# Performance work log

Hardware: AMD Instinct MI355X
Metric: run time of the kernel (lower is better)

## Reference

```python
import jax, jax.numpy as jnp
import numpy as np

EPS = 1e-12  # torch F.normalize eps

N, C, H, W = 64, 512, 40, 40
K = 64  # num_clusters


def setup_inputs() -> dict:
    key = jax.random.key(0)
    k1, k2, k3 = jax.random.split(key, 3)
    x = jax.random.normal(k1, (N, C, H, W), dtype=jnp.float32)
    conv_w = jax.random.normal(k2, (K, C, 1, 1), dtype=jnp.float32) * 0.05
    centroids = jax.random.uniform(k3, (K, C), dtype=jnp.float32)
    return {"x": x, "conv_w": conv_w, "centroids": centroids}


def _l2norm(v, axis):
    return v / jnp.maximum(jnp.sqrt(jnp.sum(v * v, axis=axis, keepdims=True)), EPS)


def reference(x, conv_w, centroids):
    n, c = x.shape[:2]
    k = conv_w.shape[0]
    # descriptor-wise L2 normalization over channels
    xn = _l2norm(x, axis=1)
    xf = xn.reshape(n, c, -1)  # [N, C, P]
    # 1x1 conv (no bias, vladv2=False) == per-pixel matmul with [K, C]
    logits = jnp.einsum('kc,ncp->nkp', conv_w.reshape(k, c), xf)
    a = jax.nn.softmax(logits, axis=1)  # soft assignment over clusters
    # VLAD: sum_p a[n,k,p] * (x[n,:,p] - centroid[k])  (weights are all-ones)
    vlad = jnp.einsum('nkp,ncp->nkc', a, xf) - a.sum(axis=-1)[:, :, None] * centroids[None]
    # intra-normalization over C, flatten, global L2 norm
    vlad = _l2norm(vlad, axis=2).reshape(n, -1)
    vlad = _l2norm(vlad, axis=1)
    return vlad
```

## Files before the change

kernel.cpp:

```cpp
#include <hip/hip_runtime.h>
#include <math.h>

#define EPSF 1e-12f


typedef short bf16x8 __attribute__((ext_vector_type(8)));
typedef float f32x4  __attribute__((ext_vector_type(4)));

__device__ __forceinline__ ushort f2b(float x) {
    unsigned u = __float_as_uint(x);
    return (ushort)((u + 0x7fffu + ((u >> 16) & 1u)) >> 16);
}

__global__ __launch_bounds__(256) void k0_wb(const float* __restrict__ W,
                                             ushort* __restrict__ Wb) {
    int i = blockIdx.x * 256 + threadIdx.x;
    if (i < 64 * 512) Wb[i] = f2b(W[i]);
}

__global__ __launch_bounds__(256) void k1_transpose(const float* __restrict__ x,
                                                    ushort* __restrict__ xbt,
                                                    float* __restrict__ rn) {
    const int n = blockIdx.y, p0 = blockIdx.x * 16;
    const int tid = threadIdx.x;
    __shared__ float tile[512 * 17];
    __shared__ float ssred[16 * 17];
    {
        const int cr = tid >> 2, pc4 = tid & 3;
        const float* src = x + ((size_t)n * 512 + cr) * 1600 + p0 + pc4 * 4;
        #pragma unroll
        for (int it = 0; it < 8; it++) {
            float4 v = *(const float4*)(src + (size_t)it * 64 * 1600);
            float* d = &tile[(cr + it * 64) * 17 + pc4 * 4];
            d[0] = v.x; d[1] = v.y; d[2] = v.z; d[3] = v.w;
        }
    }
    __syncthreads();
    {
        const int pl = tid >> 4, cc = tid & 15;
        float ss = 0.f;
        ushort buf[32] __attribute__((aligned(16)));
        #pragma unroll
        for (int i = 0; i < 32; i++) {
            float v = tile[(cc * 32 + i) * 17 + pl];
            ss = fmaf(v, v, ss);
            buf[i] = f2b(v);
        }
        ushort* dst = xbt + ((size_t)n * 1600 + p0 + pl) * 512 + cc * 32;
        #pragma unroll
        for (int ch = 0; ch < 4; ch++)
            ((uint4*)dst)[ch] = ((const uint4*)buf)[ch];
        ssred[pl * 17 + cc] = ss;
    }
    __syncthreads();
    if (tid < 16) {
        float s = 0.f;
        #pragma unroll
        for (int i = 0; i < 16; i++) s += ssred[tid * 17 + i];
        rn[n * 1600 + p0 + tid] = 1.f / fmaxf(sqrtf(s), EPSF);
    }
}

__global__ __launch_bounds__(256) void k2a_gemm1(const ushort* __restrict__ xbt,
                                                 const ushort* __restrict__ Wb,
                                                 const float* __restrict__ rn,
                                                 ushort* __restrict__ a_t,
                                                 float* __restrict__ asum) {
    const int n = blockIdx.y;
    const int p0 = blockIdx.x * 64;
    const int wv = threadIdx.x >> 6, lane = threadIdx.x & 63;
    const int q = lane >> 4, l15 = lane & 15;
    const int pw = p0 + wv * 16;

    const ushort* arow = xbt + ((size_t)n * 1600 + pw + l15) * 512 + q * 8;
    const ushort* brow = Wb + l15 * 512 + q * 8;

    f32x4 acc[4] = {};
    for (int kc = 0; kc < 512; kc += 32) {
        bf16x8 af = *(const bf16x8*)(arow + kc);
        #pragma unroll
        for (int nt = 0; nt < 4; nt++) {
            bf16x8 bf = *(const bf16x8*)(brow + nt * 16 * 512 + kc);
            acc[nt] = __builtin_amdgcn_mfma_f32_16x16x32_bf16(af, bf, acc[nt], 0, 0, 0);
        }
    }

    float rnv[4];
    #pragma unroll
    for (int r = 0; r < 4; r++) rnv[r] = rn[n * 1600 + pw + q * 4 + r];

    float v[4][4];
    float mx[4] = {-3.4e38f, -3.4e38f, -3.4e38f, -3.4e38f};
    #pragma unroll
    for (int nt = 0; nt < 4; nt++)
        #pragma unroll
        for (int r = 0; r < 4; r++) {
            v[nt][r] = acc[nt][r] * rnv[r];
            mx[r] = fmaxf(mx[r], v[nt][r]);
        }
    #pragma unroll
    for (int s = 1; s <= 8; s <<= 1)
        #pragma unroll
        for (int r = 0; r < 4; r++) mx[r] = fmaxf(mx[r], __shfl_xor(mx[r], s, 64));
    float sm[4] = {0.f, 0.f, 0.f, 0.f};
    #pragma unroll
    for (int nt = 0; nt < 4; nt++)
        #pragma unroll
        for (int r = 0; r < 4; r++) { v[nt][r] = __expf(v[nt][r] - mx[r]); sm[r] += v[nt][r]; }
    #pragma unroll
    for (int s = 1; s <= 8; s <<= 1)
        #pragma unroll
        for (int r = 0; r < 4; r++) sm[r] += __shfl_xor(sm[r], s, 64);
    float inv[4];
    #pragma unroll
    for (int r = 0; r < 4; r++) inv[r] = 1.f / sm[r];
    #pragma unroll
    for (int nt = 0; nt < 4; nt++)
        #pragma unroll
        for (int r = 0; r < 4; r++) v[nt][r] *= inv[r];

    #pragma unroll
    for (int nt = 0; nt < 4; nt++) {
        float t = v[nt][0] + v[nt][1] + v[nt][2] + v[nt][3];
        t += __shfl_xor(t, 16, 64);
        t += __shfl_xor(t, 32, 64);
        if (lane < 16) atomicAdd(&asum[n * 64 + nt * 16 + lane], t);
    }

    __shared__ ushort abuf[4][64 * 24];
    #pragma unroll
    for (int nt = 0; nt < 4; nt++)
        #pragma unroll
        for (int r = 0; r < 4; r++)
            abuf[wv][(nt * 16 + l15) * 24 + q * 4 + r] = f2b(v[nt][r] * rnv[r]);
    __syncthreads();
    ushort* dst = a_t + ((size_t)n * 64 + lane) * 1600 + pw;
    const ushort* srcl = &abuf[wv][lane * 24];
    *(uint4*)(dst)     = *(const uint4*)(srcl);
    *(uint4*)(dst + 8) = *(const uint4*)(srcl + 8);
}

__global__ __launch_bounds__(256) void k3_gemm2(const ushort* __restrict__ a_t,
                                                const float* __restrict__ x,
                                                float* __restrict__ out) {
    const int n = blockIdx.y;
    const int c0 = blockIdx.x * 256;
    const int p0 = blockIdx.z * 320;
    const int wv = threadIdx.x >> 6, lane = threadIdx.x & 63;
    const int q = lane >> 4, l15 = lane & 15;
    const int cw = c0 + wv * 64;

    const ushort* abase = a_t + ((size_t)n * 64 + l15) * 1600 + p0 + q * 8;
    const float*  xbase = x + ((size_t)n * 512 + cw + l15) * 1600 + p0 + q * 8;

    f32x4 acc[4][4] = {};
    for (int pc = 0; pc < 320; pc += 32) {
        bf16x8 af[4];
        #pragma unroll
        for (int mt = 0; mt < 4; mt++)
            af[mt] = *(const bf16x8*)(abase + (size_t)mt * 16 * 1600 + pc);
        bf16x8 bf[4];
        #pragma unroll
        for (int nt = 0; nt < 4; nt++) {
            const float* xr = xbase + (size_t)nt * 16 * 1600 + pc;
            float4 f0 = *(const float4*)(xr);
            float4 f1 = *(const float4*)(xr + 4);
            bf16x8 b;
            b[0] = (short)f2b(f0.x); b[1] = (short)f2b(f0.y);
            b[2] = (short)f2b(f0.z); b[3] = (short)f2b(f0.w);
            b[4] = (short)f2b(f1.x); b[5] = (short)f2b(f1.y);
            b[6] = (short)f2b(f1.z); b[7] = (short)f2b(f1.w);
            bf[nt] = b;
        }
        #pragma unroll
        for (int mt = 0; mt < 4; mt++)
            #pragma unroll
            for (int nt = 0; nt < 4; nt++)
                acc[mt][nt] = __builtin_amdgcn_mfma_f32_16x16x32_bf16(af[mt], bf[nt], acc[mt][nt], 0, 0, 0);
    }
    float* ob = out + (size_t)n * 32768 + cw + l15;
    #pragma unroll
    for (int mt = 0; mt < 4; mt++)
        #pragma unroll
        for (int nt = 0; nt < 4; nt++)
            #pragma unroll
            for (int r = 0; r < 4; r++)
                atomicAdd(ob + (mt * 16 + q * 4 + r) * 512 + nt * 16, acc[mt][nt][r]);
}

__global__ __launch_bounds__(256) void k4a_rownorm(const float* __restrict__ vraw,
                                                   const float* __restrict__ asum,
                                                   const float* __restrict__ cent,
                                                   float* __restrict__ rn2) {
    int row  = blockIdx.x * 4 + (threadIdx.x >> 6);
    int lane = threadIdx.x & 63;
    int k = row & 63;
    const float4* vp = (const float4*)(vraw + (size_t)row * 512 + lane * 8);
    const float4* cp = (const float4*)(cent + k * 512 + lane * 8);
    float as = asum[row];
    float4 v0 = vp[0], v1 = vp[1], c0 = cp[0], c1 = cp[1];
    float s = 0.f, t;
    t = v0.x - as * c0.x; s = fmaf(t, t, s);
    t = v0.y - as * c0.y; s = fmaf(t, t, s);
    t = v0.z - as * c0.z; s = fmaf(t, t, s);
    t = v0.w - as * c0.w; s = fmaf(t, t, s);
    t = v1.x - as * c1.x; s = fmaf(t, t, s);
    t = v1.y - as * c1.y; s = fmaf(t, t, s);
    t = v1.z - as * c1.z; s = fmaf(t, t, s);
    t = v1.w - as * c1.w; s = fmaf(t, t, s);
    #pragma unroll
    for (int off = 32; off > 0; off >>= 1) s += __shfl_down(s, off, 64);
    if (lane == 0) rn2[row] = s;
}

__global__ __launch_bounds__(64) void k4b_gn(const float* __restrict__ rn2,
                                             float* __restrict__ gn) {
    int n = blockIdx.x, k = threadIdx.x;
    float t = rn2[n * 64 + k];
    float d = fmaxf(sqrtf(t), EPSF);
    float r = t / (d * d);
    #pragma unroll
    for (int off = 32; off > 0; off >>= 1) r += __shfl_down(r, off, 64);
    if (k == 0) gn[n] = fmaxf(sqrtf(r), EPSF);
}

__global__ __launch_bounds__(256) void k4c_final(float* __restrict__ vout,
                                                 const float* __restrict__ asum,
                                                 const float* __restrict__ cent,
                                                 const float* __restrict__ rn2,
                                                 const float* __restrict__ gn) {
    int gid = blockIdx.x * 256 + threadIdx.x;
    int idx4 = gid * 4;
    int row = idx4 >> 9;
    int n = row >> 6, k = row & 63, c = idx4 & 511;
    float4 v  = *(const float4*)(vout + idx4);
    float4 cv = *(const float4*)(cent + k * 512 + c);
    float as = asum[row];
    float inv = 1.f / (fmaxf(sqrtf(rn2[row]), EPSF) * gn[n]);
    v.x = (v.x - as * cv.x) * inv;
    v.y = (v.y - as * cv.y) * inv;
    v.z = (v.z - as * cv.z) * inv;
    v.w = (v.w - as * cv.w) * inv;
    *(float4*)(vout + idx4) = v;
}

extern "C" void kernel_launch(void* const* d_in, const int* in_sizes, int n_in,
                              void* d_out, int out_size, void* d_ws, size_t ws_size,
                              hipStream_t stream) {
    const float* x    = (const float*)d_in[0];
    const float* W    = (const float*)d_in[1];
    const float* cent = (const float*)d_in[2];
    float* out = (float*)d_out;
    char* ws = (char*)d_ws;

    ushort* a_t  = (ushort*)(ws + 0);
    ushort* xbt  = (ushort*)(ws + 13107200);
    ushort* Wb   = (ushort*)(ws + 117964800);
    float*  rn   = (float*)(ws + 118030336);
    float*  asum = (float*)(ws + 118439936);
    float*  rn2  = (float*)(ws + 118456320);
    float*  gn   = (float*)(ws + 118472704);

    hipMemsetAsync(asum, 0, 64 * 64 * sizeof(float), stream);
    hipMemsetAsync(d_out, 0, (size_t)out_size * sizeof(float), stream);

    hipLaunchKernelGGL(k0_wb,       dim3(128),        dim3(256), 0, stream, W, Wb);
    hipLaunchKernelGGL(k1_transpose, dim3(100, 64),   dim3(256), 0, stream, x, xbt, rn);
    hipLaunchKernelGGL(k2a_gemm1,   dim3(25, 64),     dim3(256), 0, stream, xbt, Wb, rn, a_t, asum);
    hipLaunchKernelGGL(k3_gemm2,    dim3(2, 64, 5),   dim3(256), 0, stream, a_t, x, out);
    hipLaunchKernelGGL(k4a_rownorm, dim3(1024),       dim3(256), 0, stream, out, asum, cent, rn2);
    hipLaunchKernelGGL(k4b_gn,      dim3(64),         dim3(64),  0, stream, rn2, gn);
    hipLaunchKernelGGL(k4c_final,   dim3(2048),       dim3(256), 0, stream, out, asum, cent, rn2, gn);
}
```

Baseline: 461.0 us.

## Fuse transpose, normalization, softmax GEMM and VLAD GEMM into one kernel

Replaces the transpose, first GEMM and second GEMM kernels with one fused kernel. Each block loads a 320-pixel slab of x in 64-pixel chunks, converts them to bf16 in double-buffered shared memory, and computes per-pixel norms, logits, softmax and the assignment-weighted accumulation on-chip. This removes the bf16 transposed copy of x, the a_t buffer and their global round trips. The cost is only 320 blocks with large LDS and a 128-register accumulator array per thread, so occupancy and parallelism are low.

```diff
diff --git a/kernel.cpp b/kernel.cpp
--- a/kernel.cpp
+++ b/kernel.cpp
@@ -10,6 +10,9 @@
 __device__ __forceinline__ ushort f2b(float x) {
     unsigned u = __float_as_uint(x);
     return (ushort)((u + 0x7fffu + ((u >> 16) & 1u)) >> 16);
+}
+__device__ __forceinline__ float b2f(ushort h) {
+    return __uint_as_float(((unsigned)h) << 16);
 }
 
 __global__ __launch_bounds__(256) void k0_wb(const float* __restrict__ W,
@@ -18,174 +21,176 @@
     if (i < 64 * 512) Wb[i] = f2b(W[i]);
 }
 
-__global__ __launch_bounds__(256) void k1_transpose(const float* __restrict__ x,
-                                                    ushort* __restrict__ xbt,
-                                                    float* __restrict__ rn) {
-    const int n = blockIdx.y, p0 = blockIdx.x * 16;
+#define XSTR 72
+
+__global__ __launch_bounds__(256, 1) void k_fused(const float* __restrict__ x,
+                                                  const ushort* __restrict__ Wb,
+                                                  float* __restrict__ out,
+                                                  float* __restrict__ asum) {
+    const int n  = blockIdx.y;
+    const int p0 = blockIdx.x * 320;
     const int tid = threadIdx.x;
-    __shared__ float tile[512 * 17];
-    __shared__ float ssred[16 * 17];
+    const int wv = tid >> 6, lane = tid & 63;
+    const int q = lane >> 4, l15 = lane & 15;
+
+    __shared__ ushort xs[2][512 * XSTR] __attribute__((aligned(16)));
+    __shared__ ushort as_[64 * XSTR]    __attribute__((aligned(16)));
+
+    const int srow = tid >> 2;
+    const int spo  = (tid & 3) * 16;
+    const float* xg = x + ((size_t)(n * 512 + srow) * 1600) + p0 + spo;
+
+    f32x4 acc2[32] = {};
+    float asum_acc[4] = {0.f, 0.f, 0.f, 0.f};
+
     {
-        const int cr = tid >> 2, pc4 = tid & 3;
-        const float* src = x + ((size_t)n * 512 + cr) * 1600 + p0 + pc4 * 4;
+        float4 fr[8][4];
+        #pragma unroll
+        for (int it = 0; it < 8; it++)
+            #pragma unroll
+            for (int u = 0; u < 4; u++)
+                fr[it][u] = *(const float4*)(xg + (size_t)it * 64 * 1600 + u * 4);
         #pragma unroll
         for (int it = 0; it < 8; it++) {
-            float4 v = *(const float4*)(src + (size_t)it * 64 * 1600);
-            float* d = &tile[(cr + it * 64) * 17 + pc4 * 4];
-            d[0] = v.x; d[1] = v.y; d[2] = v.z; d[3] = v.w;
+            ushort h[16] __attribute__((aligned(16)));
+            #pragma unroll
+            for (int u = 0; u < 4; u++) {
+                h[u * 4 + 0] = f2b(fr[it][u].x);
+                h[u * 4 + 1] = f2b(fr[it][u].y);
+                h[u * 4 + 2] = f2b(fr[it][u].z);
+                h[u * 4 + 3] = f2b(fr[it][u].w);
+            }
+            ushort* d = &xs[0][(it * 64 + srow) * XSTR + spo];
+            ((uint4*)d)[0] = ((const uint4*)h)[0];
+            ((uint4*)d)[1] = ((const uint4*)h)[1];
         }
     }
     __syncthreads();
-    {
-        const int pl = tid >> 4, cc = tid & 15;
-        float ss = 0.f;
-        ushort buf[32] __attribute__((aligned(16)));
-        #pragma unroll
-        for (int i = 0; i < 32; i++) {
-            float v = tile[(cc * 32 + i) * 17 + pl];
-            ss = fmaf(v, v, ss);
-            buf[i] = f2b(v);
-        }
-        ushort* dst = xbt + ((size_t)n * 1600 + p0 + pl) * 512 + cc * 32;
-        #pragma unroll
-        for (int ch = 0; ch < 4; ch++)
-            ((uint4*)dst)[ch] = ((const uint4*)buf)[ch];
-        ssred[pl * 17 + cc] = ss;
+
+    for (int ch = 0; ch < 5; ch++) {
+        const int cur = ch & 1, nxt = cur ^ 1;
+
+        float4 fr[8][4];
+        if (ch < 4) {
+            #pragma unroll
+            for (int it = 0; it < 8; it++)
+                #pragma unroll
+                for (int u = 0; u < 4; u++)
+                    fr[it][u] = *(const float4*)(xg + (size_t)it * 64 * 1600 + (ch + 1) * 64 + u * 4);
+        }
+
+        const ushort* xcur = xs[cur];
+        const int pl = wv * 16 + l15;
+        f32x4 acc1[4] = {};
+        float ssp = 0.f;
+        for (int kc = 0; kc < 16; kc++) {
+            bf16x8 af;
+            #pragma unroll
+            for (int j = 0; j < 8; j++) {
+                ushort h = xcur[(kc * 32 + q * 8 + j) * XSTR + pl];
+                af[j] = (short)h;
+                float f = b2f(h);
+                ssp = fmaf(f, f, ssp);
+            }
+            #pragma unroll
+            for (int nt = 0; nt < 4; nt++) {
+                bf16x8 bw = *(const bf16x8*)(Wb + (nt * 16 + l15) * 512 + kc * 32 + q * 8);
+                acc1[nt] = __builtin_amdgcn_mfma_f32_16x16x32_bf16(af, bw, acc1[nt], 0, 0, 0);
+            }
+        }
+        ssp += __shfl_xor(ssp, 16, 64);
+        ssp += __shfl_xor(ssp, 32, 64);
+        float rn_l = 1.f / fmaxf(sqrtf(ssp), EPSF);
+        float rnv[4];
+        #pragma unroll
+        for (int r = 0; r < 4; r++) rnv[r] = __shfl(rn_l, q * 4 + r, 64);
+
+        float v[4][4];
+        float mx[4] = {-3.4e38f, -3.4e38f, -3.4e38f, -3.4e38f};
+        #pragma unroll
+        for (int nt = 0; nt < 4; nt++)
+            #pragma unroll
+            for (int r = 0; r < 4; r++) {
+                v[nt][r] = acc1[nt][r] * rnv[r];
+                mx[r] = fmaxf(mx[r], v[nt][r]);
+            }
+        #pragma unroll
+        for (int s = 1; s <= 8; s <<= 1)
+            #pragma unroll
+            for (int r = 0; r < 4; r++) mx[r] = fmaxf(mx[r], __shfl_xor(mx[r], s, 64));
+        float sm[4] = {0.f, 0.f, 0.f, 0.f};
+        #pragma unroll
+        for (int nt = 0; nt < 4; nt++)
+            #pragma unroll
+            for (int r = 0; r < 4; r++) { v[nt][r] = __expf(v[nt][r] - mx[r]); sm[r] += v[nt][r]; }
+        #pragma unroll
+        for (int s = 1; s <= 8; s <<= 1)
+            #pragma unroll
+            for (int r = 0; r < 4; r++) sm[r] += __shfl_xor(sm[r], s, 64);
+        float inv[4];
+        #pragma unroll
+        for (int r = 0; r < 4; r++) inv[r] = 1.f / sm[r];
+        #pragma unroll
+        for (int nt = 0; nt < 4; nt++)
+            #pragma unroll
+            for (int r = 0; r < 4; r++) v[nt][r] *= inv[r];
+
+        #pragma unroll
+        for (int nt = 0; nt < 4; nt++) {
+            float t = v[nt][0] + v[nt][1] + v[nt][2] + v[nt][3];
+            t += __shfl_xor(t, 16, 64);
+            t += __shfl_xor(t, 32, 64);
+            asum_acc[nt] += t;
+        }
+
+        #pragma unroll
+        for (int nt = 0; nt < 4; nt++)
+            #pragma unroll
+            for (int r = 0; r < 4; r++)
+                as_[(nt * 16 + l15) * XSTR + wv * 16 + q * 4 + r] = f2b(v[nt][r] * rnv[r]);
+
+        __syncthreads();
+
+        #pragma unroll
+        for (int kc = 0; kc < 2; kc++) {
+            bf16x8 afr = *(const bf16x8*)(as_ + (wv * 16 + l15) * XSTR + kc * 32 + q * 8);
+            #pragma unroll
+            for (int nt = 0; nt < 32; nt++) {
+                bf16x8 b = *(const bf16x8*)(xcur + (nt * 16 + l15) * XSTR + kc * 32 + q * 8);
+                acc2[nt] = __builtin_amdgcn_mfma_f32_16x16x32_bf16(afr, b, acc2[nt], 0, 0, 0);
+            }
+        }
+
+        if (ch < 4) {
+            #pragma unroll
+            for (int it = 0; it < 8; it++) {
+                ushort h[16] __attribute__((aligned(16)));
+                #pragma unroll
+                for (int u = 0; u < 4; u++) {
+                    h[u * 4 + 0] = f2b(fr[it][u].x);
+                    h[u * 4 + 1] = f2b(fr[it][u].y);
+                    h[u * 4 + 2] = f2b(fr[it][u].z);
+                    h[u * 4 + 3] = f2b(fr[it][u].w);
+                }
+                ushort* d = &xs[nxt][(it * 64 + srow) * XSTR + spo];
+                ((uint4*)d)[0] = ((const uint4*)h)[0];
+                ((uint4*)d)[1] = ((const uint4*)h)[1];
+            }
+        }
+        __syncthreads();
     }
-    __syncthreads();
-    if (tid < 16) {
-        float s = 0.f;
-        #pragma unroll
-        for (int i = 0; i < 16; i++) s += ssred[tid * 17 + i];
-        rn[n * 1600 + p0 + tid] = 1.f / fmaxf(sqrtf(s), EPSF);
+
+    if (lane < 16) {
+        #pragma unroll
+        for (int nt = 0; nt < 4; nt++)
+            atomicAdd(&asum[n * 64 + nt * 16 + l15], asum_acc[nt]);
     }
-}
-
-__global__ __launch_bounds__(256) void k2a_gemm1(const ushort* __restrict__ xbt,
-                                                 const ushort* __restrict__ Wb,
-                                                 const float* __restrict__ rn,
-                                                 ushort* __restrict__ a_t,
-                                                 float* __restrict__ asum) {
-    const int n = blockIdx.y;
-    const int p0 = blockIdx.x * 64;
-    const int wv = threadIdx.x >> 6, lane = threadIdx.x & 63;
-    const int q = lane >> 4, l15 = lane & 15;
-    const int pw = p0 + wv * 16;
-
-    const ushort* arow = xbt + ((size_t)n * 1600 + pw + l15) * 512 + q * 8;
-    const ushort* brow = Wb + l15 * 512 + q * 8;
-
-    f32x4 acc[4] = {};
-    for (int kc = 0; kc < 512; kc += 32) {
-        bf16x8 af = *(const bf16x8*)(arow + kc);
-        #pragma unroll
-        for (int nt = 0; nt < 4; nt++) {
-            bf16x8 bf = *(const bf16x8*)(brow + nt * 16 * 512 + kc);
-            acc[nt] = __builtin_amdgcn_mfma_f32_16x16x32_bf16(af, bf, acc[nt], 0, 0, 0);
-        }
-    }
-
-    float rnv[4];
+    float* ob = out + (size_t)n * 32768 + l15;
     #pragma unroll
-    for (int r = 0; r < 4; r++) rnv[r] = rn[n * 1600 + pw + q * 4 + r];
-
-    float v[4][4];
-    float mx[4] = {-3.4e38f, -3.4e38f, -3.4e38f, -3.4e38f};
-    #pragma unroll
-    for (int nt = 0; nt < 4; nt++)
-        #pragma unroll
-        for (int r = 0; r < 4; r++) {
-            v[nt][r] = acc[nt][r] * rnv[r];
-            mx[r] = fmaxf(mx[r], v[nt][r]);
-        }
-    #pragma unroll
-    for (int s = 1; s <= 8; s <<= 1)
-        #pragma unroll
-        for (int r = 0; r < 4; r++) mx[r] = fmaxf(mx[r], __shfl_xor(mx[r], s, 64));
-    float sm[4] = {0.f, 0.f, 0.f, 0.f};
-    #pragma unroll
-    for (int nt = 0; nt < 4; nt++)
-        #pragma unroll
-        for (int r = 0; r < 4; r++) { v[nt][r] = __expf(v[nt][r] - mx[r]); sm[r] += v[nt][r]; }
-    #pragma unroll
-    for (int s = 1; s <= 8; s <<= 1)
-        #pragma unroll
-        for (int r = 0; r < 4; r++) sm[r] += __shfl_xor(sm[r], s, 64);
-    float inv[4];
-    #pragma unroll
-    for (int r = 0; r < 4; r++) inv[r] = 1.f / sm[r];
-    #pragma unroll
-    for (int nt = 0; nt < 4; nt++)
-        #pragma unroll
-        for (int r = 0; r < 4; r++) v[nt][r] *= inv[r];
-
-    #pragma unroll
-    for (int nt = 0; nt < 4; nt++) {
-        float t = v[nt][0] + v[nt][1] + v[nt][2] + v[nt][3];
-        t += __shfl_xor(t, 16, 64);
-        t += __shfl_xor(t, 32, 64);
-        if (lane < 16) atomicAdd(&asum[n * 64 + nt * 16 + lane], t);
-    }
-
-    __shared__ ushort abuf[4][64 * 24];
-    #pragma unroll
-    for (int nt = 0; nt < 4; nt++)
+    for (int nt = 0; nt < 32; nt++)
         #pragma unroll
         for (int r = 0; r < 4; r++)
-            abuf[wv][(nt * 16 + l15) * 24 + q * 4 + r] = f2b(v[nt][r] * rnv[r]);
-    __syncthreads();
-    ushort* dst = a_t + ((size_t)n * 64 + lane) * 1600 + pw;
-    const ushort* srcl = &abuf[wv][lane * 24];
-    *(uint4*)(dst)     = *(const uint4*)(srcl);
-    *(uint4*)(dst + 8) = *(const uint4*)(srcl + 8);
-}
-
-__global__ __launch_bounds__(256) void k3_gemm2(const ushort* __restrict__ a_t,
-                                                const float* __restrict__ x,
-                                                float* __restrict__ out) {
-    const int n = blockIdx.y;
-    const int c0 = blockIdx.x * 256;
-    const int p0 = blockIdx.z * 320;
-    const int wv = threadIdx.x >> 6, lane = threadIdx.x & 63;
-    const int q = lane >> 4, l15 = lane & 15;
-    const int cw = c0 + wv * 64;
-
-    const ushort* abase = a_t + ((size_t)n * 64 + l15) * 1600 + p0 + q * 8;
-    const float*  xbase = x + ((size_t)n * 512 + cw + l15) * 1600 + p0 + q * 8;
-
-    f32x4 acc[4][4] = {};
-    for (int pc = 0; pc < 320; pc += 32) {
-        bf16x8 af[4];
-        #pragma unroll
-        for (int mt = 0; mt < 4; mt++)
-            af[mt] = *(const bf16x8*)(abase + (size_t)mt * 16 * 1600 + pc);
-        bf16x8 bf[4];
-        #pragma unroll
-        for (int nt = 0; nt < 4; nt++) {
-            const float* xr = xbase + (size_t)nt * 16 * 1600 + pc;
-            float4 f0 = *(const float4*)(xr);
-            float4 f1 = *(const float4*)(xr + 4);
-            bf16x8 b;
-            b[0] = (short)f2b(f0.x); b[1] = (short)f2b(f0.y);
-            b[2] = (short)f2b(f0.z); b[3] = (short)f2b(f0.w);
-            b[4] = (short)f2b(f1.x); b[5] = (short)f2b(f1.y);
-            b[6] = (short)f2b(f1.z); b[7] = (short)f2b(f1.w);
-            bf[nt] = b;
-        }
-        #pragma unroll
-        for (int mt = 0; mt < 4; mt++)
-            #pragma unroll
-            for (int nt = 0; nt < 4; nt++)
-                acc[mt][nt] = __builtin_amdgcn_mfma_f32_16x16x32_bf16(af[mt], bf[nt], acc[mt][nt], 0, 0, 0);
-    }
-    float* ob = out + (size_t)n * 32768 + cw + l15;
-    #pragma unroll
-    for (int mt = 0; mt < 4; mt++)
-        #pragma unroll
-        for (int nt = 0; nt < 4; nt++)
-            #pragma unroll
-            for (int r = 0; r < 4; r++)
-                atomicAdd(ob + (mt * 16 + q * 4 + r) * 512 + nt * 16, acc[mt][nt][r]);
+            atomicAdd(ob + (wv * 16 + q * 4 + r) * 512 + nt * 16, acc2[nt][r]);
 }
 
 __global__ __launch_bounds__(256) void k4a_rownorm(const float* __restrict__ vraw,
@@ -253,22 +258,17 @@
     float* out = (float*)d_out;
     char* ws = (char*)d_ws;
 
-    ushort* a_t  = (ushort*)(ws + 0);
-    ushort* xbt  = (ushort*)(ws + 13107200);
-    ushort* Wb   = (ushort*)(ws + 117964800);
-    float*  rn   = (float*)(ws + 118030336);
-    float*  asum = (float*)(ws + 118439936);
-    float*  rn2  = (float*)(ws + 118456320);
-    float*  gn   = (float*)(ws + 118472704);
+    ushort* Wb   = (ushort*)(ws + 0);
+    float*  asum = (float*)(ws + 65536);
+    float*  rn2  = (float*)(ws + 81920);
+    float*  gn   = (float*)(ws + 98304);
 
     hipMemsetAsync(asum, 0, 64 * 64 * sizeof(float), stream);
     hipMemsetAsync(d_out, 0, (size_t)out_size * sizeof(float), stream);
 
-    hipLaunchKernelGGL(k0_wb,       dim3(128),        dim3(256), 0, stream, W, Wb);
-    hipLaunchKernelGGL(k1_transpose, dim3(100, 64),   dim3(256), 0, stream, x, xbt, rn);
-    hipLaunchKernelGGL(k2a_gemm1,   dim3(25, 64),     dim3(256), 0, stream, xbt, Wb, rn, a_t, asum);
-    hipLaunchKernelGGL(k3_gemm2,    dim3(2, 64, 5),   dim3(256), 0, stream, a_t, x, out);
-    hipLaunchKernelGGL(k4a_rownorm, dim3(1024),       dim3(256), 0, stream, out, asum, cent, rn2);
-    hipLaunchKernelGGL(k4b_gn,      dim3(64),         dim3(64),  0, stream, rn2, gn);
-    hipLaunchKernelGGL(k4c_final,   dim3(2048),       dim3(256), 0, stream, out, asum, cent, rn2, gn);
-}
+    hipLaunchKernelGGL(k0_wb,       dim3(128),     dim3(256), 0, stream, W, Wb);
+    hipLaunchKernelGGL(k_fused,     dim3(5, 64),   dim3(256), 0, stream, x, Wb, out, asum);
+    hipLaunchKernelGGL(k4a_rownorm, dim3(1024),    dim3(256), 0, stream, out, asum, cent, rn2);
+    hipLaunchKernelGGL(k4b_gn,      dim3(64),      dim3(64),  0, stream, rn2, gn);
+    hipLaunchKernelGGL(k4c_final,   dim3(2048),    dim3(256), 0, stream, out, asum, cent, rn2, gn);
+}
```

Measured after the change: 474.1 us. 1.03x slower.

## Fuse transpose and L2-norm into first GEMM reading fp32 input directly

Applied to the files above, without the earlier changes.

Removes the separate transpose kernel that wrote a bf16 transposed copy of x and per-pixel inverse norms. The first GEMM now loads fp32 x directly in channel-strided form, converts it to bf16 in registers, and computes the per-pixel sum of squares with lane shuffles. This cuts a full write and re-read of an intermediate tensor, at the cost of less coalesced strided global loads in the GEMM.

```diff
diff --git a/kernel.cpp b/kernel.cpp
--- a/kernel.cpp
+++ b/kernel.cpp
@@ -18,52 +18,8 @@
     if (i < 64 * 512) Wb[i] = f2b(W[i]);
 }
 
-__global__ __launch_bounds__(256) void k1_transpose(const float* __restrict__ x,
-                                                    ushort* __restrict__ xbt,
-                                                    float* __restrict__ rn) {
-    const int n = blockIdx.y, p0 = blockIdx.x * 16;
-    const int tid = threadIdx.x;
-    __shared__ float tile[512 * 17];
-    __shared__ float ssred[16 * 17];
-    {
-        const int cr = tid >> 2, pc4 = tid & 3;
-        const float* src = x + ((size_t)n * 512 + cr) * 1600 + p0 + pc4 * 4;
-        #pragma unroll
-        for (int it = 0; it < 8; it++) {
-            float4 v = *(const float4*)(src + (size_t)it * 64 * 1600);
-            float* d = &tile[(cr + it * 64) * 17 + pc4 * 4];
-            d[0] = v.x; d[1] = v.y; d[2] = v.z; d[3] = v.w;
-        }
-    }
-    __syncthreads();
-    {
-        const int pl = tid >> 4, cc = tid & 15;
-        float ss = 0.f;
-        ushort buf[32] __attribute__((aligned(16)));
-        #pragma unroll
-        for (int i = 0; i < 32; i++) {
-            float v = tile[(cc * 32 + i) * 17 + pl];
-            ss = fmaf(v, v, ss);
-            buf[i] = f2b(v);
-        }
-        ushort* dst = xbt + ((size_t)n * 1600 + p0 + pl) * 512 + cc * 32;
-        #pragma unroll
-        for (int ch = 0; ch < 4; ch++)
-            ((uint4*)dst)[ch] = ((const uint4*)buf)[ch];
-        ssred[pl * 17 + cc] = ss;
-    }
-    __syncthreads();
-    if (tid < 16) {
-        float s = 0.f;
-        #pragma unroll
-        for (int i = 0; i < 16; i++) s += ssred[tid * 17 + i];
-        rn[n * 1600 + p0 + tid] = 1.f / fmaxf(sqrtf(s), EPSF);
-    }
-}
-
-__global__ __launch_bounds__(256) void k2a_gemm1(const ushort* __restrict__ xbt,
+__global__ __launch_bounds__(256) void k2g_gemm1(const float* __restrict__ x,
                                                  const ushort* __restrict__ Wb,
-                                                 const float* __restrict__ rn,
                                                  ushort* __restrict__ a_t,
                                                  float* __restrict__ asum) {
     const int n = blockIdx.y;
@@ -72,22 +28,33 @@
     const int q = lane >> 4, l15 = lane & 15;
     const int pw = p0 + wv * 16;
 
-    const ushort* arow = xbt + ((size_t)n * 1600 + pw + l15) * 512 + q * 8;
+    const float* xq = x + (size_t)n * 512 * 1600 + (size_t)q * 8 * 1600 + pw + l15;
     const ushort* brow = Wb + l15 * 512 + q * 8;
 
     f32x4 acc[4] = {};
-    for (int kc = 0; kc < 512; kc += 32) {
-        bf16x8 af = *(const bf16x8*)(arow + kc);
+    float ssp = 0.f;
+    for (int kc = 0; kc < 16; kc++) {
+        float fv[8];
+        #pragma unroll
+        for (int j = 0; j < 8; j++) fv[j] = xq[(size_t)(kc * 32 + j) * 1600];
+        bf16x8 af;
+        #pragma unroll
+        for (int j = 0; j < 8; j++) {
+            ssp = fmaf(fv[j], fv[j], ssp);
+            af[j] = (short)f2b(fv[j]);
+        }
         #pragma unroll
         for (int nt = 0; nt < 4; nt++) {
-            bf16x8 bf = *(const bf16x8*)(brow + nt * 16 * 512 + kc);
-            acc[nt] = __builtin_amdgcn_mfma_f32_16x16x32_bf16(af, bf, acc[nt], 0, 0, 0);
+            bf16x8 bw = *(const bf16x8*)(brow + nt * 16 * 512 + kc * 32);
+            acc[nt] = __builtin_amdgcn_mfma_f32_16x16x32_bf16(af, bw, acc[nt], 0, 0, 0);
         }
     }
-
+    ssp += __shfl_xor(ssp, 16, 64);
+    ssp += __shfl_xor(ssp, 32, 64);
+    float rn_l = 1.f / fmaxf(sqrtf(ssp), EPSF);
     float rnv[4];
     #pragma unroll
-    for (int r = 0; r < 4; r++) rnv[r] = rn[n * 1600 + pw + q * 4 + r];
+    for (int r = 0; r < 4; r++) rnv[r] = __shfl(rn_l, q * 4 + r, 64);
 
     float v[4][4];
     float mx[4] = {-3.4e38f, -3.4e38f, -3.4e38f, -3.4e38f};
@@ -254,21 +221,18 @@
     char* ws = (char*)d_ws;
 
     ushort* a_t  = (ushort*)(ws + 0);
-    ushort* xbt  = (ushort*)(ws + 13107200);
-    ushort* Wb   = (ushort*)(ws + 117964800);
-    float*  rn   = (float*)(ws + 118030336);
-    float*  asum = (float*)(ws + 118439936);
-    float*  rn2  = (float*)(ws + 118456320);
-    float*  gn   = (float*)(ws + 118472704);
+    ushort* Wb   = (ushort*)(ws + 13107200);
+    float*  asum = (float*)(ws + 13172736);
+    float*  rn2  = (float*)(ws + 13189120);
+    float*  gn   = (float*)(ws + 13205504);
 
     hipMemsetAsync(asum, 0, 64 * 64 * sizeof(float), stream);
     hipMemsetAsync(d_out, 0, (size_t)out_size * sizeof(float), stream);
 
-    hipLaunchKernelGGL(k0_wb,       dim3(128),        dim3(256), 0, stream, W, Wb);
-    hipLaunchKernelGGL(k1_transpose, dim3(100, 64),   dim3(256), 0, stream, x, xbt, rn);
-    hipLaunchKernelGGL(k2a_gemm1,   dim3(25, 64),     dim3(256), 0, stream, xbt, Wb, rn, a_t, asum);
-    hipLaunchKernelGGL(k3_gemm2,    dim3(2, 64, 5),   dim3(256), 0, stream, a_t, x, out);
-    hipLaunchKernelGGL(k4a_rownorm, dim3(1024),       dim3(256), 0, stream, out, asum, cent, rn2);
-    hipLaunchKernelGGL(k4b_gn,      dim3(64),         dim3(64),  0, stream, rn2, gn);
-    hipLaunchKernelGGL(k4c_final,   dim3(2048),       dim3(256), 0, stream, out, asum, cent, rn2, gn);
-}
+    hipLaunchKernelGGL(k0_wb,       dim3(128),      dim3(256), 0, stream, W, Wb);
+    hipLaunchKernelGGL(k2g_gemm1,   dim3(25, 64),   dim3(256), 0, stream, x, Wb, a_t, asum);
+    hipLaunchKernelGGL(k3_gemm2,    dim3(2, 64, 5), dim3(256), 0, stream, a_t, x, out);
+    hipLaunchKernelGGL(k4a_rownorm, dim3(1024),     dim3(256), 0, stream, out, asum, cent, rn2);
+    hipLaunchKernelGGL(k4b_gn,      dim3(64),       dim3(64),  0, stream, rn2, gn);
+    hipLaunchKernelGGL(k4c_final,   dim3(2048),     dim3(256), 0, stream, out, asum, cent, rn2, gn);
+}
```

Result: faster. 401.2 us (-13.0%).
